# Kernel optimization log

Measured on AMD Instinct MI355X. Metric: run time of the kernel, lower is better.

The kernel has to match this reference:

```python
import jax, jax.numpy as jnp
import numpy as np
from jax import lax

SEQ_LEN, BATCH, POSE, H, PRED_LEN = 32, 32768, 34, 16, 15


def setup_inputs() -> dict:
    key = jax.random.key(0)
    ks = jax.random.split(key, 22)
    w = lambda k, s: (jax.random.normal(k, s, jnp.float32) * 0.1)
    return {
        "obs_s": jax.random.normal(ks[0], (SEQ_LEN, BATCH, POSE), jnp.float32),
        "enc_Wih": w(ks[1], (4 * H, POSE)), "enc_Whh": w(ks[2], (4 * H, H)),
        "enc_bih": w(ks[3], (4 * H,)), "enc_bhh": w(ks[4], (4 * H,)),
        "dec_Wih": w(ks[5], (4 * H, POSE)), "dec_Whh": w(ks[6], (4 * H, H)),
        "dec_bih": w(ks[7], (4 * H,)), "dec_bhh": w(ks[8], (4 * H,)),
        "cr_Wih": w(ks[9], (4 * H, POSE)), "cr_Whh": w(ks[10], (4 * H, H)),
        "cr_bih": w(ks[11], (4 * H,)), "cr_bhh": w(ks[12], (4 * H,)),
        "fc_W": w(ks[13], (POSE, H)), "fc_b": w(ks[14], (POSE,)),
        "fcc_W": w(ks[15], (2, H)), "fcc_b": w(ks[16], (2,)),
        "mlp_W": w(ks[17], (H, H)), "mlp_b": w(ks[18], (H,)),
        "emb_W": w(ks[19], (POSE, 2)), "emb_b": w(ks[20], (POSE,)),
        "pred_len": PRED_LEN,
    }


def _cell(x, h, c, Wih, Whh, bih, bhh):
    # torch LSTM gate order: i, f, g, o
    gates = x @ Wih.T + bih + h @ Whh.T + bhh  # [B, 4H]
    i, f, g, o = jnp.split(gates, 4, axis=-1)
    c = jax.nn.sigmoid(f) * c + jax.nn.sigmoid(i) * jnp.tanh(g)
    h = jax.nn.sigmoid(o) * jnp.tanh(c)
    return h, c


def reference(obs_s, enc_Wih, enc_Whh, enc_bih, enc_bhh,
              dec_Wih, dec_Whh, dec_bih, dec_bhh,
              cr_Wih, cr_Whh, cr_bih, cr_bhh,
              fc_W, fc_b, fcc_W, fcc_b, mlp_W, mlp_b, emb_W, emb_b,
              pred_len):
    batch = obs_s.shape[1]
    h0 = jnp.zeros((batch, H), obs_s.dtype)
    c0 = jnp.zeros((batch, H), obs_s.dtype)

    def enc_step(carry, x):
        h, c = _cell(x, *carry, enc_Wih, enc_Whh, enc_bih, enc_bhh)
        return (h, c), None

    (h, c), _ = lax.scan(enc_step, (h0, c0), obs_s)

    hc = h @ mlp_W.T + mlp_b           # crossing hidden init from encoder h
    cc = jnp.zeros_like(hc)
    last_s = obs_s[-1]                 # [B, POSE]
    last_cr = obs_s[-1]

    def dec_step(carry, _):
        h, c, hc, cc, last_s, last_cr = carry
        hc, cc = _cell(last_cr, hc, cc, cr_Wih, cr_Whh, cr_bih, cr_bhh)
        curr_cr = jax.nn.softmax(hc @ fcc_W.T + fcc_b, axis=-1)   # [B, 2]
        next_cr = curr_cr @ emb_W.T + emb_b                        # [B, POSE]
        h, c = _cell(last_s, h, c, dec_Wih, dec_Whh, dec_bih, dec_bhh)
        curr_s = h @ fc_W.T + fc_b                                 # [B, POSE]
        return (h, c, hc, cc, curr_s, next_cr), (curr_s, curr_cr)

    _, (pred_s, pred_crossing) = lax.scan(
        dec_step, (h, c, hc, cc, last_s, last_cr), None, length=pred_len)
    return pred_s, pred_crossing
```

## Files before the change

### kernel.cpp

```cpp
#include <hip/hip_runtime.h>
#include <cstddef>

#define SEQLEN 32
#define BATCH  32768
#define POSE   34
#define PREDL  15
#define LOG2E  1.4426950408889634f
#define K2E    2.8853901817779268f

typedef __attribute__((ext_vector_type(8))) short short8;
typedef __attribute__((ext_vector_type(4))) float f32x4;
typedef union { short8 s8; unsigned u[4]; } pk8;

#define MF(a,b,c) __builtin_amdgcn_mfma_f32_16x16x32_bf16(a,b,c,0,0,0)
#define EXP2(x)  __builtin_amdgcn_exp2f(x)
#define RCP(x)   __builtin_amdgcn_rcpf(x)

__device__ __forceinline__ unsigned short f2bf(float f){ __bf16 b=(__bf16)f; return __builtin_bit_cast(unsigned short,b); }
__device__ __forceinline__ unsigned f22bf(float lo,float hi){ return (unsigned)f2bf(lo) | ((unsigned)f2bf(hi)<<16); }
__device__ __forceinline__ short8 zero8(){ pk8 r; r.u[0]=0;r.u[1]=0;r.u[2]=0;r.u[3]=0; return r.s8; }
__device__ __forceinline__ float scGT(int gt){ return (gt==2)?K2E:LOG2E; }

__device__ __forceinline__ short8 g8s(const float* __restrict__ p, float s){
    pk8 r;
    r.u[0]=f22bf(p[0]*s,p[1]*s); r.u[1]=f22bf(p[2]*s,p[3]*s);
    r.u[2]=f22bf(p[4]*s,p[5]*s); r.u[3]=f22bf(p[6]*s,p[7]*s);
    return r.s8;
}

__device__ __forceinline__ void pw4(const f32x4 (&ac)[4], float (&cs)[4],
                                    unsigned &hp0, unsigned &hp1){
    float hv[4];
#pragma unroll
    for(int j=0;j<4;++j){
        float A=EXP2(-ac[0][j]);
        float C=EXP2(-ac[1][j]);
        float B=EXP2( ac[2][j]);
        float O=EXP2(-ac[3][j]);
        float u=1.f+A, w=1.f+C, v=B+1.f, Bm=B-1.f;
        float t1=u*v;
        float num=fmaf(cs[j], t1, Bm*w);
        float cn=num*RCP(t1*w);
        cs[j]=cn;
        float E=EXP2(K2E*cn);
        hv[j]=(E-1.f)*RCP((1.f+O)*(E+1.f));
    }
    hp0=f22bf(hv[0],hv[1]); hp1=f22bf(hv[2],hv[3]);
}

extern "C" __global__ void lstm_prep(
    const float* __restrict__ dWih, const float* __restrict__ dWhh,
    const float* __restrict__ dbih, const float* __restrict__ dbhh,
    const float* __restrict__ cWih, const float* __restrict__ cWhh,
    const float* __restrict__ cbih, const float* __restrict__ cbhh,
    const float* __restrict__ fcW,  const float* __restrict__ fcb,
    const float* __restrict__ embW, const float* __restrict__ embb,
    float* __restrict__ wsBD, float* __restrict__ wsBC,
    unsigned short* __restrict__ wsDh, unsigned short* __restrict__ wsCh,
    unsigned short* __restrict__ wsCp)
{
    int idx = blockIdx.x*256 + threadIdx.x;
    if(idx < 1024){
        int R=idx>>4, k=idx&15;
        float s=scGT(R>>4);
        float vD=dWhh[R*16+k];
        for(int p=0;p<34;++p) vD=fmaf(dWih[R*34+p],fcW[p*16+k],vD);
        wsDh[idx]=f2bf(vD*s);
        wsCh[idx]=f2bf(cWhh[R*16+k]*s);
    }
    if(idx < 128){
        int R=idx>>1, k=idx&1;
        float s=scGT(R>>4);
        float v=0.f;
        for(int p=0;p<34;++p) v=fmaf(cWih[R*34+p],embW[2*p+k],v);
        wsCp[idx]=f2bf(v*s);
    }
    if(idx < 64){
        int R=idx;
        float s=scGT(R>>4);
        float vD=dbih[R]+dbhh[R], vC=cbih[R]+cbhh[R];
        for(int p=0;p<34;++p){ vD=fmaf(dWih[R*34+p],fcb[p],vD); vC=fmaf(cWih[R*34+p],embb[p],vC); }
        wsBD[idx]=vD*s; wsBC[idx]=vC*s;
    }
}

extern "C" __global__ void __launch_bounds__(256,2) lstm_w4(
    const float* __restrict__ obs_s,
    const float* __restrict__ eWih, const float* __restrict__ eWhh,
    const float* __restrict__ ebih, const float* __restrict__ ebhh,
    const float* __restrict__ dWih, const float* __restrict__ dWhh,
    const float* __restrict__ dbih, const float* __restrict__ dbhh,
    const float* __restrict__ cWih, const float* __restrict__ cWhh,
    const float* __restrict__ cbih, const float* __restrict__ cbhh,
    const float* __restrict__ fcW,  const float* __restrict__ fcb,
    const float* __restrict__ fccW, const float* __restrict__ fccb,
    const float* __restrict__ mlpW, const float* __restrict__ mlpb,
    const float* __restrict__ wsBD, const float* __restrict__ wsBC,
    const unsigned short* __restrict__ wsDh, const unsigned short* __restrict__ wsCh,
    const unsigned short* __restrict__ wsCp,
    float* __restrict__ out_s, float* __restrict__ out_cr)
{
    __shared__ unsigned xt4[4][4][320];

    const int tid=threadIdx.x;
    const int l=tid&63;
    const int wv=tid>>6;
    const int lo=l&15, g=l>>4;
    const int pb=blockIdx.x*64 + wv*16;
    unsigned* XT=&xt4[wv][0][0];

    unsigned pofs[5]; int wofs[5];
#pragma unroll
    for(int it=0; it<5; ++it){
        int i2=l+64*it;
        int r=i2/17, w=i2-r*17;
        pofs[it]=(unsigned)((pb+r)*17+w);
        wofs[it]=r*20+w;
    }

    short8 wEx[4], wEhT[4]; f32x4 biasE[4];
#pragma unroll
    for(int gt=0;gt<4;++gt){
        float s=scGT(gt);
        int R=gt*16+lo;
        wEx[gt]=g8s(&eWih[R*34+8*g], s);
        pk8 r2;
        r2.u[0]=f22bf(eWhh[R*16+4*g]*s,   eWhh[R*16+4*g+1]*s);
        r2.u[1]=f22bf(eWhh[R*16+4*g+2]*s, eWhh[R*16+4*g+3]*s);
        r2.u[2]=(g==0)? f22bf(eWih[R*34+32]*s, eWih[R*34+33]*s) : 0u;
        r2.u[3]=0u;
        wEhT[gt]=r2.s8;
        float4 ba=*(const float4*)&ebih[gt*16+4*g];
        float4 bb=*(const float4*)&ebhh[gt*16+4*g];
        biasE[gt]=f32x4{(ba.x+bb.x)*s,(ba.y+bb.y)*s,(ba.z+bb.z)*s,(ba.w+bb.w)*s};
    }

    float cS[4]={0.f,0.f,0.f,0.f};
    unsigned hp0=0u, hp1=0u;

    float2 RA[4][5], RB[4][5];
    auto ldblk=[&](float2 (&R)[4][5], int t0){
#pragma unroll
        for(int s=0;s<4;++s){
            const float2* base=(const float2*)obs_s + (size_t)(t0+s)*(BATCH*17);
#pragma unroll
            for(int it=0;it<5;++it)
                if(it<4 || l<16) R[s][it]=base[pofs[it]];
        }
    };
    auto wrblk=[&](const float2 (&R)[4][5]){
#pragma unroll
        for(int s=0;s<4;++s)
#pragma unroll
            for(int it=0;it<5;++it)
                if(it<4 || l<16) XT[s*320+wofs[it]]=f22bf(R[s][it].x,R[s][it].y);
    };
    auto rdfrag=[&](int s, short8 &b, unsigned &tw){
        b=*(const short8*)&XT[s*320+lo*20+4*g];
        tw=XT[s*320+lo*20+16];
    };
    auto enc_compute=[&](short8 b0, unsigned tw){
        pk8 bh; bh.u[0]=hp0; bh.u[1]=hp1; bh.u[2]=(g==0)?tw:0u; bh.u[3]=0u;
        f32x4 acc[4];
#pragma unroll
        for(int gt=0;gt<4;++gt){
            f32x4 cx=MF(wEx[gt], b0, biasE[gt]);
            acc[gt]=MF(wEhT[gt], bh.s8, cx);
        }
        pw4(acc, cS, hp0, hp1);
    };

    short8 fbQ=zero8(); unsigned ftQ=0u;
    ldblk(RA,0);
    ldblk(RB,4);
#pragma unroll
    for(int kb=0;kb<8;++kb){
        if(kb&1){ wrblk(RB); if(kb+2<8) ldblk(RB,4*(kb+2)); }
        else    { wrblk(RA); if(kb+2<8) ldblk(RA,4*(kb+2)); }
        short8 fb; unsigned ft;
        rdfrag(0,fb,ft);
#pragma unroll
        for(int i=0;i<4;++i){
            short8 nfb=zero8(); unsigned nft=0u;
            if(i<3) rdfrag(i+1,nfb,nft);
            if(kb==7 && i==3){ fbQ=fb; ftQ=ft; }
            enc_compute(fb,ft);
            fb=nfb; ft=nft;
        }
    }

    short8 wDh[4], wCA[4]; f32x4 biasD[4], biasC[4];
#pragma unroll
    for(int gt=0;gt<4;++gt){
        int R=gt*16+lo;
        uint2 qd=*(const uint2*)&wsDh[R*16+4*g];
        pk8 rd; rd.u[0]=qd.x; rd.u[1]=qd.y; rd.u[2]=0u; rd.u[3]=0u;
        wDh[gt]=rd.s8;
        uint2 qc=*(const uint2*)&wsCh[R*16+4*g];
        pk8 rc; rc.u[0]=qc.x; rc.u[1]=qc.y;
        rc.u[2]=(g==0)? *(const unsigned*)&wsCp[R*2] : 0u; rc.u[3]=0u;
        wCA[gt]=rc.s8;
        biasD[gt]=*(const f32x4*)&wsBD[gt*16+4*g];
        biasC[gt]=*(const f32x4*)&wsBC[gt*16+4*g];
    }
    short8 wF[3]; f32x4 fcbF[3];
#pragma unroll
    for(int nt=0;nt<3;++nt){
        int np=nt*16+lo;
        if(np<POSE){
            pk8 r;
            r.u[0]=f22bf(fcW[np*16+4*g],   fcW[np*16+4*g+1]);
            r.u[1]=f22bf(fcW[np*16+4*g+2], fcW[np*16+4*g+3]);
            r.u[2]=0u; r.u[3]=0u;
            wF[nt]=r.s8;
        } else wF[nt]=zero8();
#pragma unroll
        for(int j=0;j<4;++j){
            int row=nt*16+4*g+j;
            fcbF[nt][j]=(row<POSE)? fcb[row] : 0.f;
        }
    }
    short8 wFC, wM; f32x4 fccC, mlpbF;
    if(lo<2){
        pk8 r;
        r.u[0]=f22bf(fccW[lo*16+4*g],   fccW[lo*16+4*g+1]);
        r.u[1]=f22bf(fccW[lo*16+4*g+2], fccW[lo*16+4*g+3]);
        r.u[2]=0u; r.u[3]=0u; wFC=r.s8;
    } else wFC=zero8();
    fccC=(g==0)? f32x4{fccb[0],fccb[1],0.f,0.f} : f32x4{0.f,0.f,0.f,0.f};
    {
        pk8 r;
        r.u[0]=f22bf(mlpW[lo*16+4*g],   mlpW[lo*16+4*g+1]);
        r.u[1]=f22bf(mlpW[lo*16+4*g+2], mlpW[lo*16+4*g+3]);
        r.u[2]=0u; r.u[3]=0u; wM=r.s8;
        mlpbF=*(const f32x4*)&mlpb[4*g];
    }

    unsigned hcp0,hcp1;
    {
        pk8 bh; bh.u[0]=hp0; bh.u[1]=hp1; bh.u[2]=0u; bh.u[3]=0u;
        f32x4 o=MF(wM,bh.s8,mlpbF);
        hcp0=f22bf(o[0],o[1]); hcp1=f22bf(o[2],o[3]);
    }
    float cC[4]={0.f,0.f,0.f,0.f};
    unsigned pp=0u;

    auto dec_tail=[&](int s, const f32x4 (&aC)[4], const f32x4 (&aD)[4]){
        pw4(aD,cS,hp0,hp1);
        pw4(aC,cC,hcp0,hcp1);
        pk8 bhc; bhc.u[0]=hcp0; bhc.u[1]=hcp1; bhc.u[2]=0u; bhc.u[3]=0u;
        f32x4 zz=MF(wFC,bhc.s8,fccC);
        float z0=zz[0], z1=zz[1];
        float mx=fmaxf(z0,z1);
        float e0=EXP2(LOG2E*(z0-mx)), e1=EXP2(LOG2E*(z1-mx));
        float rs=RCP(e0+e1);
        float p0=e0*rs, p1=e1*rs;
        unsigned ppn=f22bf(p0,p1);
        if(g==0)
            ((float2*)out_cr)[(size_t)s*BATCH+pb+lo]=make_float2(p0,p1);
        pp=(unsigned)__shfl((int)ppn, lo, 64);
        pk8 bh; bh.u[0]=hp0; bh.u[1]=hp1; bh.u[2]=0u; bh.u[3]=0u;
        float* po = out_s + ((size_t)s*BATCH + pb + lo)*POSE;
        f32x4 o0=MF(wF[0],bh.s8,fcbF[0]);
        f32x4 o1=MF(wF[1],bh.s8,fcbF[1]);
        *(float2*)(po+4*g)     =make_float2(o0[0],o0[1]);
        *(float2*)(po+4*g+2)   =make_float2(o0[2],o0[3]);
        *(float2*)(po+16+4*g)  =make_float2(o1[0],o1[1]);
        *(float2*)(po+16+4*g+2)=make_float2(o1[2],o1[3]);
        f32x4 o2=MF(wF[2],bh.s8,fcbF[2]);
        if(g==0) *(float2*)(po+32)=make_float2(o2[0],o2[1]);
    };

    {
        f32x4 aC[4], aD[4];
#pragma unroll
        for(int gt=0;gt<4;++gt){
            float s=scGT(gt);
            int R=gt*16+lo;
            short8 a1=g8s(&cWih[R*34+8*g], s);
            pk8 a2;
            a2.u[0]=f22bf(cWhh[R*16+4*g]*s,   cWhh[R*16+4*g+1]*s);
            a2.u[1]=f22bf(cWhh[R*16+4*g+2]*s, cWhh[R*16+4*g+3]*s);
            a2.u[2]=(g==0)? f22bf(cWih[R*34+32]*s, cWih[R*34+33]*s) : 0u;
            a2.u[3]=0u;
            float4 ba=*(const float4*)&cbih[gt*16+4*g];
            float4 bb=*(const float4*)&cbhh[gt*16+4*g];
            f32x4 bc0={(ba.x+bb.x)*s,(ba.y+bb.y)*s,(ba.z+bb.z)*s,(ba.w+bb.w)*s};
            pk8 bhc; bhc.u[0]=hcp0; bhc.u[1]=hcp1; bhc.u[2]=(g==0)?ftQ:0u; bhc.u[3]=0u;
            f32x4 cx=MF(a1,fbQ,bc0);
            aC[gt]=MF(a2.s8,bhc.s8,cx);
            short8 d1=g8s(&dWih[R*34+8*g], s);
            pk8 d2;
            d2.u[0]=f22bf(dWhh[R*16+4*g]*s,   dWhh[R*16+4*g+1]*s);
            d2.u[1]=f22bf(dWhh[R*16+4*g+2]*s, dWhh[R*16+4*g+3]*s);
            d2.u[2]=(g==0)? f22bf(dWih[R*34+32]*s, dWih[R*34+33]*s) : 0u;
            d2.u[3]=0u;
            float4 da=*(const float4*)&dbih[gt*16+4*g];
            float4 db=*(const float4*)&dbhh[gt*16+4*g];
            f32x4 bd0={(da.x+db.x)*s,(da.y+db.y)*s,(da.z+db.z)*s,(da.w+db.w)*s};
            pk8 bhd; bhd.u[0]=hp0; bhd.u[1]=hp1; bhd.u[2]=(g==0)?ftQ:0u; bhd.u[3]=0u;
            f32x4 dx=MF(d1,fbQ,bd0);
            aD[gt]=MF(d2.s8,bhd.s8,dx);
        }
        dec_tail(0,aC,aD);
    }
    for(int s=1;s<PREDL;++s){
        pk8 bd; bd.u[0]=hp0; bd.u[1]=hp1; bd.u[2]=0u; bd.u[3]=0u;
        pk8 bc; bc.u[0]=hcp0; bc.u[1]=hcp1; bc.u[2]=(g==0)?pp:0u; bc.u[3]=0u;
        f32x4 aC[4], aD[4];
#pragma unroll
        for(int gt=0;gt<4;++gt) aD[gt]=MF(wDh[gt],bd.s8,biasD[gt]);
#pragma unroll
        for(int gt=0;gt<4;++gt) aC[gt]=MF(wCA[gt],bc.s8,biasC[gt]);
        dec_tail(s,aC,aD);
    }
}

extern "C" void kernel_launch(void* const* d_in, const int* in_sizes, int n_in,
                              void* d_out, int out_size, void* d_ws, size_t ws_size,
                              hipStream_t stream)
{
    const float* obs  = (const float*)d_in[0];
    const float* eWih = (const float*)d_in[1];
    const float* eWhh = (const float*)d_in[2];
    const float* ebih = (const float*)d_in[3];
    const float* ebhh = (const float*)d_in[4];
    const float* dWih = (const float*)d_in[5];
    const float* dWhh = (const float*)d_in[6];
    const float* dbih = (const float*)d_in[7];
    const float* dbhh = (const float*)d_in[8];
    const float* cWih = (const float*)d_in[9];
    const float* cWhh = (const float*)d_in[10];
    const float* cbih = (const float*)d_in[11];
    const float* cbhh = (const float*)d_in[12];
    const float* fcW  = (const float*)d_in[13];
    const float* fcb  = (const float*)d_in[14];
    const float* fccW = (const float*)d_in[15];
    const float* fccb = (const float*)d_in[16];
    const float* mlpW = (const float*)d_in[17];
    const float* mlpb = (const float*)d_in[18];
    const float* embW = (const float*)d_in[19];
    const float* embb = (const float*)d_in[20];

    float* out_s  = (float*)d_out;
    float* out_cr = out_s + (size_t)PREDL*BATCH*POSE;

    float* wsBD = (float*)d_ws;
    float* wsBC = wsBD + 64;
    unsigned short* wsDh = (unsigned short*)(wsBC+64);
    unsigned short* wsCh = wsDh + 1024;
    unsigned short* wsCp = wsCh + 1024;

    hipLaunchKernelGGL(lstm_prep, dim3(4), dim3(256), 0, stream,
                       dWih, dWhh, dbih, dbhh, cWih, cWhh, cbih, cbhh,
                       fcW, fcb, embW, embb, wsBD, wsBC, wsDh, wsCh, wsCp);
    hipLaunchKernelGGL(lstm_w4, dim3(BATCH/64), dim3(256), 0, stream,
                       obs, eWih, eWhh, ebih, ebhh, dWih, dWhh, dbih, dbhh,
                       cWih, cWhh, cbih, cbhh, fcW, fcb, fccW, fccb,
                       mlpW, mlpb, wsBD, wsBC, wsDh, wsCh, wsCp,
                       out_s, out_cr);
}
```

Measured before the change: 68.48 us.

## Batch input-projection MFMAs per block and vectorize LSTM pointwise math

The encoder loop now issues all sixteen input-projection MFMAs for a 4-step block before the dependent recurrent MFMAs, taking the x-part off the serial h-dependency chain. The global-load prefetch goes from double-buffered (two register blocks, two ahead) to single-buffered (one ahead), freeing registers for the cx accumulators. The pointwise LSTM gate math is rewritten on float4 vector types so the compiler can emit packed float ops. The cost is higher register pressure from 16 live accumulators and less load latency hiding.

```diff
diff --git a/kernel.cpp b/kernel.cpp
--- a/kernel.cpp
+++ b/kernel.cpp
@@ -28,23 +28,30 @@
     return r.s8;
 }
 
-__device__ __forceinline__ void pw4(const f32x4 (&ac)[4], float (&cs)[4],
-                                    unsigned &hp0, unsigned &hp1){
-    float hv[4];
+__device__ __forceinline__ void pw4v(const f32x4 (&ac)[4], f32x4 &cs,
+                                     unsigned &hp0, unsigned &hp1){
+    f32x4 A,C,B,O;
 #pragma unroll
     for(int j=0;j<4;++j){
-        float A=EXP2(-ac[0][j]);
-        float C=EXP2(-ac[1][j]);
-        float B=EXP2( ac[2][j]);
-        float O=EXP2(-ac[3][j]);
-        float u=1.f+A, w=1.f+C, v=B+1.f, Bm=B-1.f;
-        float t1=u*v;
-        float num=fmaf(cs[j], t1, Bm*w);
-        float cn=num*RCP(t1*w);
-        cs[j]=cn;
-        float E=EXP2(K2E*cn);
-        hv[j]=(E-1.f)*RCP((1.f+O)*(E+1.f));
-    }
+        A[j]=EXP2(-ac[0][j]); C[j]=EXP2(-ac[1][j]);
+        B[j]=EXP2( ac[2][j]); O[j]=EXP2(-ac[3][j]);
+    }
+    const f32x4 one={1.f,1.f,1.f,1.f};
+    f32x4 u=one+A, w=one+C, v=B+one, Bm=B-one;
+    f32x4 t1=u*v;
+    f32x4 num=cs*t1+Bm*w;
+    f32x4 den=t1*w;
+    f32x4 rd_,E,rh;
+#pragma unroll
+    for(int j=0;j<4;++j) rd_[j]=RCP(den[j]);
+    f32x4 cn=num*rd_;
+    cs=cn;
+#pragma unroll
+    for(int j=0;j<4;++j) E[j]=EXP2(K2E*cn[j]);
+    f32x4 hd=(one+O)*(E+one);
+#pragma unroll
+    for(int j=0;j<4;++j) rh[j]=RCP(hd[j]);
+    f32x4 hv=(E-one)*rh;
     hp0=f22bf(hv[0],hv[1]); hp1=f22bf(hv[2],hv[3]);
 }
 
@@ -84,7 +91,7 @@
     }
 }
 
-extern "C" __global__ void __launch_bounds__(256,2) lstm_w4(
+extern "C" __global__ void __launch_bounds__(256,2) lstm_w5(
     const float* __restrict__ obs_s,
     const float* __restrict__ eWih, const float* __restrict__ eWhh,
     const float* __restrict__ ebih, const float* __restrict__ ebhh,
@@ -135,10 +142,10 @@
         biasE[gt]=f32x4{(ba.x+bb.x)*s,(ba.y+bb.y)*s,(ba.z+bb.z)*s,(ba.w+bb.w)*s};
     }
 
-    float cS[4]={0.f,0.f,0.f,0.f};
+    f32x4 cS={0.f,0.f,0.f,0.f};
     unsigned hp0=0u, hp1=0u;
 
-    float2 RA[4][5], RB[4][5];
+    float2 RA[4][5];
     auto ldblk=[&](float2 (&R)[4][5], int t0){
 #pragma unroll
         for(int s=0;s<4;++s){
@@ -155,37 +162,33 @@
             for(int it=0;it<5;++it)
                 if(it<4 || l<16) XT[s*320+wofs[it]]=f22bf(R[s][it].x,R[s][it].y);
     };
-    auto rdfrag=[&](int s, short8 &b, unsigned &tw){
-        b=*(const short8*)&XT[s*320+lo*20+4*g];
-        tw=XT[s*320+lo*20+16];
-    };
-    auto enc_compute=[&](short8 b0, unsigned tw){
-        pk8 bh; bh.u[0]=hp0; bh.u[1]=hp1; bh.u[2]=(g==0)?tw:0u; bh.u[3]=0u;
-        f32x4 acc[4];
-#pragma unroll
-        for(int gt=0;gt<4;++gt){
-            f32x4 cx=MF(wEx[gt], b0, biasE[gt]);
-            acc[gt]=MF(wEhT[gt], bh.s8, cx);
-        }
-        pw4(acc, cS, hp0, hp1);
-    };
 
     short8 fbQ=zero8(); unsigned ftQ=0u;
     ldblk(RA,0);
-    ldblk(RB,4);
 #pragma unroll
     for(int kb=0;kb<8;++kb){
-        if(kb&1){ wrblk(RB); if(kb+2<8) ldblk(RB,4*(kb+2)); }
-        else    { wrblk(RA); if(kb+2<8) ldblk(RA,4*(kb+2)); }
-        short8 fb; unsigned ft;
-        rdfrag(0,fb,ft);
-#pragma unroll
-        for(int i=0;i<4;++i){
-            short8 nfb=zero8(); unsigned nft=0u;
-            if(i<3) rdfrag(i+1,nfb,nft);
-            if(kb==7 && i==3){ fbQ=fb; ftQ=ft; }
-            enc_compute(fb,ft);
-            fb=nfb; ft=nft;
+        wrblk(RA);
+        if(kb+1<8) ldblk(RA,4*(kb+1));
+        short8 bx[4]; unsigned tw[4];
+#pragma unroll
+        for(int s=0;s<4;++s){
+            bx[s]=*(const short8*)&XT[s*320+lo*20+4*g];
+            tw[s]=XT[s*320+lo*20+16];
+        }
+        f32x4 cx[4][4];
+#pragma unroll
+        for(int s=0;s<4;++s)
+#pragma unroll
+            for(int gt=0;gt<4;++gt)
+                cx[s][gt]=MF(wEx[gt],bx[s],biasE[gt]);
+        if(kb==7){ fbQ=bx[3]; ftQ=tw[3]; }
+#pragma unroll
+        for(int s=0;s<4;++s){
+            pk8 bh; bh.u[0]=hp0; bh.u[1]=hp1; bh.u[2]=(g==0)?tw[s]:0u; bh.u[3]=0u;
+            f32x4 acc[4];
+#pragma unroll
+            for(int gt=0;gt<4;++gt) acc[gt]=MF(wEhT[gt],bh.s8,cx[s][gt]);
+            pw4v(acc,cS,hp0,hp1);
         }
     }
 
@@ -242,12 +245,12 @@
         f32x4 o=MF(wM,bh.s8,mlpbF);
         hcp0=f22bf(o[0],o[1]); hcp1=f22bf(o[2],o[3]);
     }
-    float cC[4]={0.f,0.f,0.f,0.f};
+    f32x4 cC={0.f,0.f,0.f,0.f};
     unsigned pp=0u;
 
     auto dec_tail=[&](int s, const f32x4 (&aC)[4], const f32x4 (&aD)[4]){
-        pw4(aD,cS,hp0,hp1);
-        pw4(aC,cC,hcp0,hcp1);
+        pw4v(aD,cS,hp0,hp1);
+        pw4v(aC,cC,hcp0,hcp1);
         pk8 bhc; bhc.u[0]=hcp0; bhc.u[1]=hcp1; bhc.u[2]=0u; bhc.u[3]=0u;
         f32x4 zz=MF(wFC,bhc.s8,fccC);
         float z0=zz[0], z1=zz[1];
@@ -354,7 +357,7 @@
     hipLaunchKernelGGL(lstm_prep, dim3(4), dim3(256), 0, stream,
                        dWih, dWhh, dbih, dbhh, cWih, cWhh, cbih, cbhh,
                        fcW, fcb, embW, embb, wsBD, wsBC, wsDh, wsCh, wsCp);
-    hipLaunchKernelGGL(lstm_w4, dim3(BATCH/64), dim3(256), 0, stream,
+    hipLaunchKernelGGL(lstm_w5, dim3(BATCH/64), dim3(256), 0, stream,
                        obs, eWih, eWhh, ebih, ebhh, dWih, dWhh, dbih, dbhh,
                        cWih, cWhh, cbih, cbhh, fcW, fcb, fccW, fccb,
                        mlpW, mlpb, wsBD, wsBC, wsDh, wsCh, wsCp,
```

New measurement: 64.51 us. 1.06x faster.
